# Performance work log

Measured on AMD Instinct MI355X. Metric: run time of the kernel, lower is better.

Reference implementation:

```python
import jax, jax.numpy as jnp
import numpy as np
from jax import lax

SIM_RATIO = 0.5
TAU = 1e-4
BN_EPS = 1e-5
COS_EPS = 1e-6
LEAKY_SLOPE = 0.01


def setup_inputs() -> dict:
    key = jax.random.key(0)
    ks = jax.random.split(key, 4)
    B, N, D = 2048, 50000, 128
    user_item_id = jax.random.randint(ks[0], (B, 2), 0, N, dtype=jnp.int64 if jax.config.jax_enable_x64 else jnp.int32).astype(jnp.int32)
    item_feature = jax.random.normal(ks[1], (B, 2 * D), dtype=jnp.float32)
    all_items = jax.random.normal(ks[2], (N, D), dtype=jnp.float32)
    # Linear(2D -> D) params (stored transposed: x @ W + b), BatchNorm1d affine params
    W = jax.random.normal(ks[3], (2 * D, D), dtype=jnp.float32) / np.float32(np.sqrt(2 * D))
    b = jnp.zeros((D,), jnp.float32)
    gamma = jnp.ones((D,), jnp.float32)
    beta = jnp.zeros((D,), jnp.float32)
    return {"user_item_id": user_item_id, "item_feature": item_feature,
            "all_items": all_items, "W": W, "b": b, "gamma": gamma, "beta": beta}


def _mlp(x, W, b, gamma, beta):
    # Linear + BatchNorm1d (training mode: batch stats, biased var) + LeakyReLU
    h = x @ W + b                                  # [B, D]
    mean = h.mean(axis=0)
    var = ((h - mean) ** 2).mean(axis=0)
    h = (h - mean) * lax.rsqrt(var + BN_EPS) * gamma + beta
    return jnp.where(h >= 0, h, LEAKY_SLOPE * h)


def reference(user_item_id, item_feature, all_items, W, b, gamma, beta):
    B = item_feature.shape[0]
    N = all_items.shape[0]
    h = _mlp(item_feature, W, b, gamma, beta)       # [B, D]
    scores = h @ all_items.T                         # [B, N]
    # hard gumbel-softmax, tau=1e-4
    g = jax.random.gumbel(jax.random.key(42), scores.shape, scores.dtype)
    soft = jax.nn.softmax((scores + g) / TAU, axis=-1)
    idx = jnp.argmax(soft, axis=-1)                  # [B]
    onehot = jax.nn.one_hot(idx, N, dtype=scores.dtype)
    probs = onehot + soft - lax.stop_gradient(soft)  # straight-through hard one-hot
    repl_feat = probs @ all_items                    # [B, D] (one-hot gather via matmul)
    repl_items = (jnp.arange(N, dtype=scores.dtype) * probs).sum(axis=1).astype(jnp.int32)
    orig_feat = all_items[user_item_id[:, 1]]        # [B, D]
    # cosine similarity along dim=1 with eps=1e-6 (torch semantics)
    dot = (orig_feat * repl_feat).sum(axis=1)
    n1 = jnp.maximum(jnp.linalg.norm(orig_feat, axis=1), COS_EPS)
    n2 = jnp.maximum(jnp.linalg.norm(repl_feat, axis=1), COS_EPS)
    sim = dot / (n1 * n2)
    sim = (sim + 1.0) / 2.0                          # regularize_similarity
    labels = jnp.full((B,), SIM_RATIO, dtype=sim.dtype)
    sim_loss = jnp.mean((sim - labels) ** 2)         # SimilarityMarginLoss ~ MSE to ratio
    return repl_items, sim_loss, sim.mean()
```

## Files before the change

kernel.cpp:

```cpp
#include <hip/hip_runtime.h>
#include <math.h>

#define TINYF 1.17549435e-38f
#define GMAX 16.0f
#define NTILES 1563
#define TPB 25

typedef __attribute__((ext_vector_type(8))) short bf16x8;
typedef __attribute__((ext_vector_type(4))) float f32x4;

__device__ __forceinline__ unsigned rotl32(unsigned x, int r) {
  return (x << r) | (x >> (32 - r));
}

__device__ __forceinline__ unsigned tf2x32_xor(unsigned x0, unsigned x1) {
  const unsigned k0 = 0u, k1 = 42u, k2 = 0x1BD11BF0u;
  x0 += k0; x1 += k1;
#define TFR(r) { x0 += x1; x1 = rotl32(x1, r); x1 ^= x0; }
  TFR(13) TFR(15) TFR(26) TFR(6)
  x0 += k1; x1 += k2 + 1u;
  TFR(17) TFR(29) TFR(16) TFR(24)
  x0 += k2; x1 += k0 + 2u;
  TFR(13) TFR(15) TFR(26) TFR(6)
  x0 += k0; x1 += k1 + 3u;
  TFR(17) TFR(29) TFR(16) TFR(24)
  x0 += k1; x1 += k2 + 4u;
  TFR(13) TFR(15) TFR(26) TFR(6)
  x0 += k2; x1 += k0 + 5u;
#undef TFR
  return x0 ^ x1;
}

__device__ __forceinline__ float gumbel_from_bits(unsigned bits) {
  float f = __uint_as_float((bits >> 9) | 0x3f800000u) - 1.0f;
  float u = fmaxf(f, TINYF);
  return -logf(-logf(u));
}

__device__ __forceinline__ unsigned ordf(float v) {
  unsigned b = __float_as_uint(v);
  return (b & 0x80000000u) ? ~b : (b | 0x80000000u);
}
__device__ __forceinline__ float unordf(unsigned u) {
  unsigned b = (u & 0x80000000u) ? (u & 0x7FFFFFFFu) : ~u;
  return __uint_as_float(b);
}

__device__ __forceinline__ unsigned short f2bf(float f) {
  unsigned u = __float_as_uint(f);
  unsigned r = u + 0x7FFFu + ((u >> 16) & 1u);
  return (unsigned short)(r >> 16);
}
__device__ __forceinline__ unsigned pk2(float a, float b) {
  return (unsigned)f2bf(a) | ((unsigned)f2bf(b) << 16);
}
__device__ __forceinline__ int bswz(int b) { return b ^ (((b >> 8) & 7) << 4); }

__device__ __attribute__((noinline)) void resolve_cand(
    int R, int J, float s, float ERRC,
    const float* __restrict__ hfin, const float* __restrict__ items,
    const float* __restrict__ V0,
    unsigned long long* __restrict__ rowslot, const volatile unsigned* hiw) {
  const unsigned hi0 = hiw[2 * R + 1];
  float tv = V0[R];
  if (hi0) tv = fmaxf(tv, unordf(hi0));
  const float thr2 = tv - ERRC;
  const float d = thr2 - s;
  const unsigned bits = tf2x32_xor(0u, (unsigned)R * 50000u + (unsigned)J);
  const float f = __uint_as_float((bits >> 9) | 0x3f800000u) - 1.0f;
  const float u = fmaxf(f, TINYF);
  const float thr_u = __expf(-__expf(-d)) * (1.0f - 2e-5f);
  if (u < thr_u) return;
  const float g = -logf(-logf(u));
  if (s + g < thr2) return;
  const float4* hp = (const float4*)(hfin + (size_t)R * 128);
  const float4* ap = (const float4*)(items + (size_t)J * 128);
  float4 a4 = {0.f, 0.f, 0.f, 0.f};
#pragma unroll
  for (int k = 0; k < 32; ++k) {
    float4 h = hp[k];
    float4 b = ap[k];
    a4.x = fmaf(h.x, b.x, a4.x);
    a4.y = fmaf(h.y, b.y, a4.y);
    a4.z = fmaf(h.z, b.z, a4.z);
    a4.w = fmaf(h.w, b.w, a4.w);
  }
  const float v = ((a4.x + a4.y) + (a4.z + a4.w)) + g;
  const unsigned ov = ordf(v);
  if (ov >= hiw[2 * R + 1]) {
    const unsigned long long pk =
        ((unsigned long long)ov << 32) | (0xFFFFFFFFu - (unsigned)J);
    atomicMax(&rowslot[R], pk);
  }
}

__global__ void k_hraw(const float* __restrict__ x, const float* __restrict__ W,
                       const float* __restrict__ b, float* __restrict__ hraw,
                       unsigned long long* __restrict__ rowslot,
                       float* __restrict__ norms) {
  __shared__ float sx[256];
  const int i = blockIdx.x;
  const int d = threadIdx.x;
  if (d == 0) {
    rowslot[i] = 0ull;
    if (i == 0) { norms[0] = 0.0f; norms[1] = 0.0f; }
  }
  sx[d] = x[i * 256 + d];
  sx[d + 128] = x[i * 256 + 128 + d];
  __syncthreads();
  double acc = 0.0;
  for (int k = 0; k < 256; ++k)
    acc = fma((double)sx[k], (double)W[k * 128 + d], acc);
  hraw[i * 128 + d] = (float)acc + b[d];
}

__global__ void k_bnstats(const float* __restrict__ hraw,
                          float* __restrict__ meanv, float* __restrict__ rsv) {
  __shared__ double red[256];
  const int d = blockIdx.x;
  const int t = threadIdx.x;
  double s = 0.0;
  for (int i = t; i < 2048; i += 256) s += (double)hraw[i * 128 + d];
  red[t] = s;
  __syncthreads();
  for (int off = 128; off > 0; off >>= 1) {
    if (t < off) red[t] += red[t + off];
    __syncthreads();
  }
  const float m = (float)(red[0] * (1.0 / 2048.0));
  __syncthreads();
  double v = 0.0;
  for (int i = t; i < 2048; i += 256) {
    float dd = __fsub_rn(hraw[i * 128 + d], m);
    v += (double)dd * (double)dd;
  }
  red[t] = v;
  __syncthreads();
  for (int off = 128; off > 0; off >>= 1) {
    if (t < off) red[t] += red[t + off];
    __syncthreads();
  }
  if (t == 0) {
    float var = (float)(red[0] * (1.0 / 2048.0));
    float vpe = __fadd_rn(var, 1e-5f);
    meanv[d] = m;
    rsv[d] = (float)(1.0 / sqrt((double)vpe));
  }
}

__global__ void k_apply(const float* __restrict__ hraw,
                        const float* __restrict__ meanv, const float* __restrict__ rsv,
                        const float* __restrict__ gamma, const float* __restrict__ beta,
                        float* __restrict__ hfin, unsigned short* __restrict__ hb,
                        float* __restrict__ norms) {
  __shared__ float red[256];
  const int t = threadIdx.x;
  const int idx = blockIdx.x * 256 + t;
  const int d = idx & 127;
  float h = hraw[idx];
  float hn = __fadd_rn(__fmul_rn(__fmul_rn(__fsub_rn(h, meanv[d]), rsv[d]), gamma[d]), beta[d]);
  float o = (hn >= 0.0f) ? hn : __fmul_rn(0.01f, hn);
  hfin[idx] = o;
  hb[idx] = f2bf(o);
  red[t] = o * o;
  __syncthreads();
  for (int off = 64; off > 0; off >>= 1) {
    if ((t & 127) < off) red[t] += red[t + off];
    __syncthreads();
  }
  if ((t & 127) == 0) atomicMax((unsigned*)&norms[0], __float_as_uint(red[t]));
}

__global__ void k_anorm(const float* __restrict__ items, float* __restrict__ norms) {
  __shared__ float red[4];
  const int t = threadIdx.x;
  int row = blockIdx.x * 32 + (t >> 3);
  if (row > 49999) row = 49999;
  const float4* p = (const float4*)(items + (size_t)row * 128 + (t & 7) * 16);
  float ss = 0.0f;
#pragma unroll
  for (int k = 0; k < 4; ++k) {
    float4 v = p[k];
    ss += v.x * v.x + v.y * v.y + v.z * v.z + v.w * v.w;
  }
  ss += __shfl_xor(ss, 1);
  ss += __shfl_xor(ss, 2);
  ss += __shfl_xor(ss, 4);
  ss = fmaxf(ss, __shfl_xor(ss, 8));
  ss = fmaxf(ss, __shfl_xor(ss, 16));
  ss = fmaxf(ss, __shfl_xor(ss, 32));
  if ((t & 63) == 0) red[t >> 6] = ss;
  __syncthreads();
  if (t == 0) {
    float mx = fmaxf(fmaxf(red[0], red[1]), fmaxf(red[2], red[3]));
    atomicMax((unsigned*)&norms[1], __float_as_uint(mx));
  }
}

__global__ __launch_bounds__(256, 4) void k_seed(const float* __restrict__ hfin,
                                                 const float* __restrict__ items,
                                                 float* __restrict__ V0) {
  __shared__ float red[4][256];
  const int t = threadIdx.x;
  const int rbase = blockIdx.x * 4;
  float best[4] = {-INFINITY, -INFINITY, -INFINITY, -INFINITY};
  for (int q = 0; q < 4; ++q) {
    const int j = t + 256 * q;
    float acc[4] = {0.0f, 0.0f, 0.0f, 0.0f};
    const float* ap = items + (size_t)j * 128;
    for (int km = 0; km < 8; ++km) {
#pragma unroll
      for (int e = 0; e < 4; ++e) {
        float4 a4 = *(const float4*)(ap + km * 16 + 4 * e);
#pragma unroll
        for (int p = 0; p < 4; ++p) {
          const float* hp = hfin + (rbase + p) * 128 + km * 16 + 4 * e;
          float4 h4 = *(const float4*)hp;
          acc[p] = fmaf(h4.x, a4.x, acc[p]);
          acc[p] = fmaf(h4.y, a4.y, acc[p]);
          acc[p] = fmaf(h4.z, a4.z, acc[p]);
          acc[p] = fmaf(h4.w, a4.w, acc[p]);
        }
      }
    }
#pragma unroll
    for (int p = 0; p < 4; ++p) {
      unsigned l = (unsigned)(rbase + p) * 50000u + (unsigned)j;
      float g = gumbel_from_bits(tf2x32_xor(0u, l));
      best[p] = fmaxf(best[p], acc[p] + g);
    }
  }
#pragma unroll
  for (int p = 0; p < 4; ++p) red[p][t] = best[p];
  __syncthreads();
  for (int off = 128; off > 0; off >>= 1) {
    if (t < off) {
#pragma unroll
      for (int p = 0; p < 4; ++p) red[p][t] = fmaxf(red[p][t], red[p][t + off]);
    }
    __syncthreads();
  }
  if (t < 4) V0[rbase + t] = red[t][0];
}

__global__ __launch_bounds__(256, 2) void k_screen(
    const unsigned short* __restrict__ hb, const float* __restrict__ hfin,
    const float* __restrict__ items, const float* __restrict__ V0,
    const float* __restrict__ norms, unsigned long long* __restrict__ rowslot) {
  __shared__ __align__(16) unsigned short Bs[2][32 * 128];
  __shared__ unsigned qk[4][128];
  __shared__ float qsh[4][128];

  const int t = threadIdx.x;
  const int w = t >> 6, l = t & 63;
  const int lg = l >> 4, lr = l & 15;
  const int rg = blockIdx.x >> 6;
  const int span = blockIdx.x & 63;
  const int r0 = rg * 128;
  const int r0w = r0 + w * 32;
  const int tile0 = span * TPB;
  int nt = NTILES - tile0;
  nt = nt < 0 ? 0 : (nt > TPB ? TPB : nt);
  if (nt == 0) return;

  const float ERRC = 0.004f * sqrtf(norms[0] * norms[1]) + 0.01f;
  const volatile unsigned* hiw = (const volatile unsigned*)rowslot;

  const unsigned short* aB0 = hb + (size_t)(r0w + lr) * 128 + lg * 8;
  bf16x8 Afrag[2][4];
#pragma unroll
  for (int kb = 0; kb < 4; ++kb) {
    Afrag[0][kb] = *(const bf16x8*)(aB0 + kb * 32);
    Afrag[1][kb] = *(const bf16x8*)(aB0 + 16 * 128 + kb * 32);
  }

  const int jl = t >> 3;
  const int c0 = (t & 7) * 16;
  float4 f0, f1, f2, f3;

  {
    const int Jg = min(tile0 * 32 + jl, 49999);
    const float4* src = (const float4*)(items + (size_t)Jg * 128 + c0);
    f0 = src[0]; f1 = src[1]; f2 = src[2]; f3 = src[3];
    uint4 A, B;
    A.x = pk2(f0.x, f0.y); A.y = pk2(f0.z, f0.w);
    A.z = pk2(f1.x, f1.y); A.w = pk2(f1.z, f1.w);
    B.x = pk2(f2.x, f2.y); B.y = pk2(f2.z, f2.w);
    B.z = pk2(f3.x, f3.y); B.w = pk2(f3.z, f3.w);
    const int byte0 = jl * 256 + c0 * 2;
    *(uint4*)((char*)Bs[0] + bswz(byte0)) = A;
    *(uint4*)((char*)Bs[0] + bswz(byte0 + 16)) = B;
  }
  if (nt > 1) {
    const int Jg = min((tile0 + 1) * 32 + jl, 49999);
    const float4* src = (const float4*)(items + (size_t)Jg * 128 + c0);
    f0 = src[0]; f1 = src[1]; f2 = src[2]; f3 = src[3];
  }
  __syncthreads();

  const unsigned long long lml = (1ull << l) - 1ull;
  unsigned qn = 0;
  float th1[2][4];

  int pb = 0;
  for (int it = 0; it < nt; ++it) {
    const int j0 = (tile0 + it) * 32;

    if ((it & 3) == 0) {
#pragma unroll
      for (int rt = 0; rt < 2; ++rt)
#pragma unroll
        for (int q = 0; q < 4; ++q) {
          const int R = r0w + rt * 16 + lg * 4 + q;
          const unsigned hi = hiw[2 * R + 1];
          float tv = V0[R];
          if (hi) tv = fmaxf(tv, unordf(hi));
          th1[rt][q] = tv - GMAX - ERRC;
        }
    }

    if (it + 1 < nt) {
      uint4 A, B;
      A.x = pk2(f0.x, f0.y); A.y = pk2(f0.z, f0.w);
      A.z = pk2(f1.x, f1.y); A.w = pk2(f1.z, f1.w);
      B.x = pk2(f2.x, f2.y); B.y = pk2(f2.z, f2.w);
      B.z = pk2(f3.x, f3.y); B.w = pk2(f3.z, f3.w);
      const int byte0 = jl * 256 + c0 * 2;
      *(uint4*)((char*)Bs[pb ^ 1] + bswz(byte0)) = A;
      *(uint4*)((char*)Bs[pb ^ 1] + bswz(byte0 + 16)) = B;
    }
    if (it + 2 < nt) {
      const int Jg = min((tile0 + it + 2) * 32 + jl, 49999);
      const float4* src = (const float4*)(items + (size_t)Jg * 128 + c0);
      f0 = src[0]; f1 = src[1]; f2 = src[2]; f3 = src[3];
    }

    f32x4 acc[2][2];
#pragma unroll
    for (int rt = 0; rt < 2; ++rt)
#pragma unroll
      for (int jt = 0; jt < 2; ++jt) acc[rt][jt] = (f32x4){0.f, 0.f, 0.f, 0.f};

#pragma unroll
    for (int kb = 0; kb < 4; ++kb) {
#pragma unroll
      for (int jt = 0; jt < 2; ++jt) {
        const int byte = (jt * 16 + lr) * 256 + kb * 64 + lg * 16;
        bf16x8 bfrag = *(const bf16x8*)((char*)Bs[pb] + bswz(byte));
        acc[0][jt] = __builtin_amdgcn_mfma_f32_16x16x32_bf16(Afrag[0][kb], bfrag, acc[0][jt], 0, 0, 0);
        acc[1][jt] = __builtin_amdgcn_mfma_f32_16x16x32_bf16(Afrag[1][kb], bfrag, acc[1][jt], 0, 0, 0);
      }
    }

#pragma unroll
    for (int rt = 0; rt < 2; ++rt)
#pragma unroll
      for (int q = 0; q < 4; ++q) {
        const float th = th1[rt][q];
#pragma unroll
        for (int jt = 0; jt < 2; ++jt) {
          const float s = acc[rt][jt][q];
          const int J = j0 + jt * 16 + lr;
          const bool c = (J < 50000) && (s >= th);
          const unsigned long long m = __ballot(c);
          if (m) {
            if (c) {
              const unsigned idx = qn + (unsigned)__popcll(m & lml);
              qk[w][idx] = ((unsigned)(rt * 16 + lg * 4 + q) << 16) | (unsigned)J;
              qsh[w][idx] = s;
            }
            qn += (unsigned)__popcll(m);
            if (qn >= 64) {
              for (unsigned i = (unsigned)l; i < qn; i += 64) {
                const unsigned key = qk[w][i];
                resolve_cand(r0w + (int)(key >> 16), (int)(key & 0xFFFFu),
                             qsh[w][i], ERRC, hfin, items, V0, rowslot, hiw);
              }
              qn = 0;
            }
          }
        }
      }

    __syncthreads();
    pb ^= 1;
  }

  for (unsigned i = (unsigned)l; i < qn; i += 64) {
    const unsigned key = qk[w][i];
    resolve_cand(r0w + (int)(key >> 16), (int)(key & 0xFFFFu),
                 qsh[w][i], ERRC, hfin, items, V0, rowslot, hiw);
  }
}

__global__ void k_final(const unsigned long long* __restrict__ rowslot,
                        const int* __restrict__ uid, const float* __restrict__ items,
                        float* __restrict__ dout, float* __restrict__ simv) {
  const int r = blockIdx.x;
  const int lane = threadIdx.x;
  const unsigned long long pk = rowslot[r];
  const int bi = (int)(0xFFFFFFFFu - (unsigned)pk);
  if (lane == 0) dout[r] = (float)bi;

  const int orig = uid[r * 2 + 1];
  float o1 = items[(size_t)orig * 128 + lane];
  float o2 = items[(size_t)orig * 128 + 64 + lane];
  float p1 = items[(size_t)bi * 128 + lane];
  float p2 = items[(size_t)bi * 128 + 64 + lane];
  float d = o1 * p1 + o2 * p2;
  float s1 = o1 * o1 + o2 * o2;
  float s2 = p1 * p1 + p2 * p2;
  for (int off = 32; off > 0; off >>= 1) {
    d += __shfl_down(d, off);
    s1 += __shfl_down(s1, off);
    s2 += __shfl_down(s2, off);
  }
  if (lane == 0) {
    float n1 = fmaxf(sqrtf(s1), 1e-6f);
    float n2 = fmaxf(sqrtf(s2), 1e-6f);
    float sim = d / (n1 * n2);
    simv[r] = (sim + 1.0f) * 0.5f;
  }
}

__global__ void k_reduce(const float* __restrict__ simv, float* __restrict__ dout) {
  __shared__ double rl[256];
  __shared__ double rs[256];
  const int t = threadIdx.x;
  double L = 0.0, S = 0.0;
  for (int i = t; i < 2048; i += 256) {
    double s = (double)simv[i];
    double dd = s - 0.5;
    L += dd * dd;
    S += s;
  }
  rl[t] = L; rs[t] = S;
  __syncthreads();
  for (int off = 128; off > 0; off >>= 1) {
    if (t < off) { rl[t] += rl[t + off]; rs[t] += rs[t + off]; }
    __syncthreads();
  }
  if (t == 0) {
    dout[2048] = (float)(rl[0] * (1.0 / 2048.0));
    dout[2049] = (float)(rs[0] * (1.0 / 2048.0));
  }
}

extern "C" void kernel_launch(void* const* d_in, const int* in_sizes, int n_in,
                              void* d_out, int out_size, void* d_ws, size_t ws_size,
                              hipStream_t stream) {
  const int* uid = (const int*)d_in[0];
  const float* xfeat = (const float*)d_in[1];
  const float* items = (const float*)d_in[2];
  const float* W = (const float*)d_in[3];
  const float* bias = (const float*)d_in[4];
  const float* gamma = (const float*)d_in[5];
  const float* beta = (const float*)d_in[6];

  float* ws = (float*)d_ws;
  float* hraw = ws;
  float* hfin = ws + 262144;
  float* meanv = ws + 524288;
  float* rsv = ws + 524416;
  float* V0 = ws + 524544;
  float* simv = ws + 526592;
  float* norms = ws + 528640;
  unsigned long long* rowslot =
      (unsigned long long*)(ws + 528642);
  unsigned short* hb = (unsigned short*)(ws + 532740);
  float* dout = (float*)d_out;

  hipLaunchKernelGGL(k_hraw, dim3(2048), dim3(128), 0, stream, xfeat, W, bias, hraw, rowslot, norms);
  hipLaunchKernelGGL(k_bnstats, dim3(128), dim3(256), 0, stream, hraw, meanv, rsv);
  hipLaunchKernelGGL(k_apply, dim3(1024), dim3(256), 0, stream, hraw, meanv, rsv, gamma, beta, hfin, hb, norms);
  hipLaunchKernelGGL(k_anorm, dim3(1563), dim3(256), 0, stream, items, norms);
  hipLaunchKernelGGL(k_seed, dim3(512), dim3(256), 0, stream, hfin, items, V0);
  hipLaunchKernelGGL(k_screen, dim3(1024), dim3(256), 0, stream, hb, hfin, items, V0, norms, rowslot);
  hipLaunchKernelGGL(k_final, dim3(2048), dim3(64), 0, stream, rowslot, uid, items, dout, simv);
  hipLaunchKernelGGL(k_reduce, dim3(1), dim3(256), 0, stream, simv, dout);
}
```

Before: 411.0 us.

## Pre-convert items to bf16 and stage screen tiles via direct global-to-LDS loads

Adds a kernel that converts the item table to bf16 once per call into workspace. The screening kernel then streams tiles with global_load_lds straight into the swizzled shared buffer, instead of loading fp32 into registers, packing, and writing to LDS. This halves the bytes streamed per tile and frees VGPRs and VALU work in the hot loop. The cost is an extra conversion pass over the 50000x128 table each call, plus a fallback path that is taken when the workspace is too small.

```diff
diff --git a/kernel.cpp b/kernel.cpp
--- a/kernel.cpp
+++ b/kernel.cpp
@@ -94,6 +94,17 @@
   }
 }
 
+__global__ void k_bconv(const float* __restrict__ items,
+                        unsigned short* __restrict__ ib) {
+  const int e = (blockIdx.x * 256 + threadIdx.x) * 8;
+  const float4 a = *(const float4*)(items + e);
+  const float4 b = *(const float4*)(items + e + 4);
+  uint4 o;
+  o.x = pk2(a.x, a.y); o.y = pk2(a.z, a.w);
+  o.z = pk2(b.x, b.y); o.w = pk2(b.z, b.w);
+  *(uint4*)(ib + e) = o;
+}
+
 __global__ void k_hraw(const float* __restrict__ x, const float* __restrict__ W,
                        const float* __restrict__ b, float* __restrict__ hraw,
                        unsigned long long* __restrict__ rowslot,
@@ -243,9 +254,10 @@
   if (t < 4) V0[rbase + t] = red[t][0];
 }
 
-__global__ __launch_bounds__(256, 2) void k_screen(
+__global__ __launch_bounds__(256, 2) void k_screen_dma(
     const unsigned short* __restrict__ hb, const float* __restrict__ hfin,
-    const float* __restrict__ items, const float* __restrict__ V0,
+    const float* __restrict__ items, const unsigned short* __restrict__ ib,
+    const float* __restrict__ V0,
     const float* __restrict__ norms, unsigned long long* __restrict__ rowslot) {
   __shared__ __align__(16) unsigned short Bs[2][32 * 128];
   __shared__ unsigned qk[4][128];
@@ -274,28 +286,26 @@
     Afrag[1][kb] = *(const bf16x8*)(aB0 + 16 * 128 + kb * 32);
   }
 
-  const int jl = t >> 3;
-  const int c0 = (t & 7) * 16;
-  float4 f0, f1, f2, f3;
-
-  {
-    const int Jg = min(tile0 * 32 + jl, 49999);
-    const float4* src = (const float4*)(items + (size_t)Jg * 128 + c0);
-    f0 = src[0]; f1 = src[1]; f2 = src[2]; f3 = src[3];
-    uint4 A, B;
-    A.x = pk2(f0.x, f0.y); A.y = pk2(f0.z, f0.w);
-    A.z = pk2(f1.x, f1.y); A.w = pk2(f1.z, f1.w);
-    B.x = pk2(f2.x, f2.y); B.y = pk2(f2.z, f2.w);
-    B.z = pk2(f3.x, f3.y); B.w = pk2(f3.z, f3.w);
-    const int byte0 = jl * 256 + c0 * 2;
-    *(uint4*)((char*)Bs[0] + bswz(byte0)) = A;
-    *(uint4*)((char*)Bs[0] + bswz(byte0 + 16)) = B;
-  }
-  if (nt > 1) {
-    const int Jg = min((tile0 + 1) * 32 + jl, 49999);
-    const float4* src = (const float4*)(items + (size_t)Jg * 128 + c0);
-    f0 = src[0]; f1 = src[1]; f2 = src[2]; f3 = src[3];
-  }
+  const int o0 = w * 2048 + l * 16;
+  const int row0 = o0 >> 8, col0 = o0 & 255;
+  const int o1 = o0 + 1024;
+  const int row1 = o1 >> 8, col1 = o1 & 255;
+  const int sc0 = col0 ^ ((row0 & 7) << 4);
+  const int sc1 = col1 ^ ((row1 & 7) << 4);
+
+#define STAGE_TILE(tl, buf)                                                    \
+  {                                                                            \
+    const int Jg0 = min((tl) * 32 + row0, 49999);                              \
+    const int Jg1 = min((tl) * 32 + row1, 49999);                              \
+    __builtin_amdgcn_global_load_lds(                                          \
+        (const unsigned int*)((const char*)ib + (size_t)Jg0 * 256 + sc0),      \
+        (unsigned int*)((char*)Bs[buf] + w * 2048), 16, 0, 0);                 \
+    __builtin_amdgcn_global_load_lds(                                          \
+        (const unsigned int*)((const char*)ib + (size_t)Jg1 * 256 + sc1),      \
+        (unsigned int*)((char*)Bs[buf] + w * 2048 + 1024), 16, 0, 0);          \
+  }
+
+  STAGE_TILE(tile0, 0)
   __syncthreads();
 
   const unsigned long long lml = (1ull << l) - 1ull;
@@ -305,6 +315,8 @@
   int pb = 0;
   for (int it = 0; it < nt; ++it) {
     const int j0 = (tile0 + it) * 32;
+
+    if (it + 1 < nt) STAGE_TILE(tile0 + it + 1, pb ^ 1)
 
     if ((it & 3) == 0) {
 #pragma unroll
@@ -317,22 +329,6 @@
           if (hi) tv = fmaxf(tv, unordf(hi));
           th1[rt][q] = tv - GMAX - ERRC;
         }
-    }
-
-    if (it + 1 < nt) {
-      uint4 A, B;
-      A.x = pk2(f0.x, f0.y); A.y = pk2(f0.z, f0.w);
-      A.z = pk2(f1.x, f1.y); A.w = pk2(f1.z, f1.w);
-      B.x = pk2(f2.x, f2.y); B.y = pk2(f2.z, f2.w);
-      B.z = pk2(f3.x, f3.y); B.w = pk2(f3.z, f3.w);
-      const int byte0 = jl * 256 + c0 * 2;
-      *(uint4*)((char*)Bs[pb ^ 1] + bswz(byte0)) = A;
-      *(uint4*)((char*)Bs[pb ^ 1] + bswz(byte0 + 16)) = B;
-    }
-    if (it + 2 < nt) {
-      const int Jg = min((tile0 + it + 2) * 32 + jl, 49999);
-      const float4* src = (const float4*)(items + (size_t)Jg * 128 + c0);
-      f0 = src[0]; f1 = src[1]; f2 = src[2]; f3 = src[3];
     }
 
     f32x4 acc[2][2];
@@ -391,6 +387,157 @@
     resolve_cand(r0w + (int)(key >> 16), (int)(key & 0xFFFFu),
                  qsh[w][i], ERRC, hfin, items, V0, rowslot, hiw);
   }
+#undef STAGE_TILE
+}
+
+__global__ __launch_bounds__(256, 2) void k_screen_reg(
+    const unsigned short* __restrict__ hb, const float* __restrict__ hfin,
+    const float* __restrict__ items, const float* __restrict__ V0,
+    const float* __restrict__ norms, unsigned long long* __restrict__ rowslot) {
+  __shared__ __align__(16) unsigned short Bs[2][32 * 128];
+  __shared__ unsigned qk[4][128];
+  __shared__ float qsh[4][128];
+
+  const int t = threadIdx.x;
+  const int w = t >> 6, l = t & 63;
+  const int lg = l >> 4, lr = l & 15;
+  const int rg = blockIdx.x >> 6;
+  const int span = blockIdx.x & 63;
+  const int r0 = rg * 128;
+  const int r0w = r0 + w * 32;
+  const int tile0 = span * TPB;
+  int nt = NTILES - tile0;
+  nt = nt < 0 ? 0 : (nt > TPB ? TPB : nt);
+  if (nt == 0) return;
+
+  const float ERRC = 0.004f * sqrtf(norms[0] * norms[1]) + 0.01f;
+  const volatile unsigned* hiw = (const volatile unsigned*)rowslot;
+
+  const unsigned short* aB0 = hb + (size_t)(r0w + lr) * 128 + lg * 8;
+  bf16x8 Afrag[2][4];
+#pragma unroll
+  for (int kb = 0; kb < 4; ++kb) {
+    Afrag[0][kb] = *(const bf16x8*)(aB0 + kb * 32);
+    Afrag[1][kb] = *(const bf16x8*)(aB0 + 16 * 128 + kb * 32);
+  }
+
+  const int jl = t >> 3;
+  const int c0 = (t & 7) * 16;
+  float4 f0, f1, f2, f3;
+
+  {
+    const int Jg = min(tile0 * 32 + jl, 49999);
+    const float4* src = (const float4*)(items + (size_t)Jg * 128 + c0);
+    f0 = src[0]; f1 = src[1]; f2 = src[2]; f3 = src[3];
+    uint4 A, B;
+    A.x = pk2(f0.x, f0.y); A.y = pk2(f0.z, f0.w);
+    A.z = pk2(f1.x, f1.y); A.w = pk2(f1.z, f1.w);
+    B.x = pk2(f2.x, f2.y); B.y = pk2(f2.z, f2.w);
+    B.z = pk2(f3.x, f3.y); B.w = pk2(f3.z, f3.w);
+    const int byte0 = jl * 256 + c0 * 2;
+    *(uint4*)((char*)Bs[0] + bswz(byte0)) = A;
+    *(uint4*)((char*)Bs[0] + bswz(byte0 + 16)) = B;
+  }
+  if (nt > 1) {
+    const int Jg = min((tile0 + 1) * 32 + jl, 49999);
+    const float4* src = (const float4*)(items + (size_t)Jg * 128 + c0);
+    f0 = src[0]; f1 = src[1]; f2 = src[2]; f3 = src[3];
+  }
+  __syncthreads();
+
+  const unsigned long long lml = (1ull << l) - 1ull;
+  unsigned qn = 0;
+  float th1[2][4];
+
+  int pb = 0;
+  for (int it = 0; it < nt; ++it) {
+    const int j0 = (tile0 + it) * 32;
+
+    if ((it & 3) == 0) {
+#pragma unroll
+      for (int rt = 0; rt < 2; ++rt)
+#pragma unroll
+        for (int q = 0; q < 4; ++q) {
+          const int R = r0w + rt * 16 + lg * 4 + q;
+          const unsigned hi = hiw[2 * R + 1];
+          float tv = V0[R];
+          if (hi) tv = fmaxf(tv, unordf(hi));
+          th1[rt][q] = tv - GMAX - ERRC;
+        }
+    }
+
+    if (it + 1 < nt) {
+      uint4 A, B;
+      A.x = pk2(f0.x, f0.y); A.y = pk2(f0.z, f0.w);
+      A.z = pk2(f1.x, f1.y); A.w = pk2(f1.z, f1.w);
+      B.x = pk2(f2.x, f2.y); B.y = pk2(f2.z, f2.w);
+      B.z = pk2(f3.x, f3.y); B.w = pk2(f3.z, f3.w);
+      const int byte0 = jl * 256 + c0 * 2;
+      *(uint4*)((char*)Bs[pb ^ 1] + bswz(byte0)) = A;
+      *(uint4*)((char*)Bs[pb ^ 1] + bswz(byte0 + 16)) = B;
+    }
+    if (it + 2 < nt) {
+      const int Jg = min((tile0 + it + 2) * 32 + jl, 49999);
+      const float4* src = (const float4*)(items + (size_t)Jg * 128 + c0);
+      f0 = src[0]; f1 = src[1]; f2 = src[2]; f3 = src[3];
+    }
+
+    f32x4 acc[2][2];
+#pragma unroll
+    for (int rt = 0; rt < 2; ++rt)
+#pragma unroll
+      for (int jt = 0; jt < 2; ++jt) acc[rt][jt] = (f32x4){0.f, 0.f, 0.f, 0.f};
+
+#pragma unroll
+    for (int kb = 0; kb < 4; ++kb) {
+#pragma unroll
+      for (int jt = 0; jt < 2; ++jt) {
+        const int byte = (jt * 16 + lr) * 256 + kb * 64 + lg * 16;
+        bf16x8 bfrag = *(const bf16x8*)((char*)Bs[pb] + bswz(byte));
+        acc[0][jt] = __builtin_amdgcn_mfma_f32_16x16x32_bf16(Afrag[0][kb], bfrag, acc[0][jt], 0, 0, 0);
+        acc[1][jt] = __builtin_amdgcn_mfma_f32_16x16x32_bf16(Afrag[1][kb], bfrag, acc[1][jt], 0, 0, 0);
+      }
+    }
+
+#pragma unroll
+    for (int rt = 0; rt < 2; ++rt)
+#pragma unroll
+      for (int q = 0; q < 4; ++q) {
+        const float th = th1[rt][q];
+#pragma unroll
+        for (int jt = 0; jt < 2; ++jt) {
+          const float s = acc[rt][jt][q];
+          const int J = j0 + jt * 16 + lr;
+          const bool c = (J < 50000) && (s >= th);
+          const unsigned long long m = __ballot(c);
+          if (m) {
+            if (c) {
+              const unsigned idx = qn + (unsigned)__popcll(m & lml);
+              qk[w][idx] = ((unsigned)(rt * 16 + lg * 4 + q) << 16) | (unsigned)J;
+              qsh[w][idx] = s;
+            }
+            qn += (unsigned)__popcll(m);
+            if (qn >= 64) {
+              for (unsigned i = (unsigned)l; i < qn; i += 64) {
+                const unsigned key = qk[w][i];
+                resolve_cand(r0w + (int)(key >> 16), (int)(key & 0xFFFFu),
+                             qsh[w][i], ERRC, hfin, items, V0, rowslot, hiw);
+              }
+              qn = 0;
+            }
+          }
+        }
+      }
+
+    __syncthreads();
+    pb ^= 1;
+  }
+
+  for (unsigned i = (unsigned)l; i < qn; i += 64) {
+    const unsigned key = qk[w][i];
+    resolve_cand(r0w + (int)(key >> 16), (int)(key & 0xFFFFu),
+                 qsh[w][i], ERRC, hfin, items, V0, rowslot, hiw);
+  }
 }
 
 __global__ void k_final(const unsigned long long* __restrict__ rowslot,
@@ -468,14 +615,22 @@
   unsigned long long* rowslot =
       (unsigned long long*)(ws + 528642);
   unsigned short* hb = (unsigned short*)(ws + 532740);
+  unsigned short* ib = (unsigned short*)(ws + 663812);
   float* dout = (float*)d_out;
 
+  const bool big_ws = ws_size >= (size_t)15455248;
+
+  if (big_ws)
+    hipLaunchKernelGGL(k_bconv, dim3(3125), dim3(256), 0, stream, items, ib);
   hipLaunchKernelGGL(k_hraw, dim3(2048), dim3(128), 0, stream, xfeat, W, bias, hraw, rowslot, norms);
   hipLaunchKernelGGL(k_bnstats, dim3(128), dim3(256), 0, stream, hraw, meanv, rsv);
   hipLaunchKernelGGL(k_apply, dim3(1024), dim3(256), 0, stream, hraw, meanv, rsv, gamma, beta, hfin, hb, norms);
   hipLaunchKernelGGL(k_anorm, dim3(1563), dim3(256), 0, stream, items, norms);
   hipLaunchKernelGGL(k_seed, dim3(512), dim3(256), 0, stream, hfin, items, V0);
-  hipLaunchKernelGGL(k_screen, dim3(1024), dim3(256), 0, stream, hb, hfin, items, V0, norms, rowslot);
+  if (big_ws)
+    hipLaunchKernelGGL(k_screen_dma, dim3(1024), dim3(256), 0, stream, hb, hfin, items, ib, V0, norms, rowslot);
+  else
+    hipLaunchKernelGGL(k_screen_reg, dim3(1024), dim3(256), 0, stream, hb, hfin, items, V0, norms, rowslot);
   hipLaunchKernelGGL(k_final, dim3(2048), dim3(64), 0, stream, rowslot, uid, items, dout, simv);
   hipLaunchKernelGGL(k_reduce, dim3(1), dim3(256), 0, stream, simv, dout);
 }
```

Measured after the change: 412.4 us. No clear change (+0.4%).

## Precast items to bf16 once and stream tiles via direct global-to-LDS loads

Applied to the files above, without the earlier changes.

Replaces the item-norm kernel with one that also writes a bf16 copy of the item table while computing the max norm. The screening kernel then loads pre-swizzled bf16 tiles straight into LDS with global_load_lds, instead of loading fp32 into registers and packing per tile. The row tile per block is halved (16 rows per wave, 64 per block) and the grid doubles, so each block does less MFMA work per B tile and thresholds are refreshed every iteration via a shuffle. This trades an extra pass writing about 12.8MB of bf16 for half the bytes read per tile and lower register pressure, but each tile is now re-read by twice as many blocks.

```diff
diff --git a/kernel.cpp b/kernel.cpp
--- a/kernel.cpp
+++ b/kernel.cpp
@@ -114,6 +114,43 @@
   hraw[i * 128 + d] = (float)acc + b[d];
 }
 
+__global__ void k_bca(const float* __restrict__ items,
+                      unsigned short* __restrict__ ib,
+                      float* __restrict__ norms) {
+  __shared__ float red[4];
+  const int t = threadIdx.x;
+  const int row = blockIdx.x * 32 + (t >> 3);
+  const int rc = row > 49999 ? 49999 : row;
+  const int c = (t & 7) * 16;
+  const float4* p = (const float4*)(items + (size_t)rc * 128 + c);
+  const float4 v0 = p[0], v1 = p[1], v2 = p[2], v3 = p[3];
+  float ss = v0.x * v0.x + v0.y * v0.y + v0.z * v0.z + v0.w * v0.w +
+             v1.x * v1.x + v1.y * v1.y + v1.z * v1.z + v1.w * v1.w +
+             v2.x * v2.x + v2.y * v2.y + v2.z * v2.z + v2.w * v2.w +
+             v3.x * v3.x + v3.y * v3.y + v3.z * v3.z + v3.w * v3.w;
+  if (row <= 49999) {
+    uint4 o0, o1;
+    o0.x = pk2(v0.x, v0.y); o0.y = pk2(v0.z, v0.w);
+    o0.z = pk2(v1.x, v1.y); o0.w = pk2(v1.z, v1.w);
+    o1.x = pk2(v2.x, v2.y); o1.y = pk2(v2.z, v2.w);
+    o1.z = pk2(v3.x, v3.y); o1.w = pk2(v3.z, v3.w);
+    uint4* dst = (uint4*)(ib + (size_t)row * 128 + c);
+    dst[0] = o0; dst[1] = o1;
+  }
+  ss += __shfl_xor(ss, 1);
+  ss += __shfl_xor(ss, 2);
+  ss += __shfl_xor(ss, 4);
+  ss = fmaxf(ss, __shfl_xor(ss, 8));
+  ss = fmaxf(ss, __shfl_xor(ss, 16));
+  ss = fmaxf(ss, __shfl_xor(ss, 32));
+  if ((t & 63) == 0) red[t >> 6] = ss;
+  __syncthreads();
+  if (t == 0) {
+    float mx = fmaxf(fmaxf(red[0], red[1]), fmaxf(red[2], red[3]));
+    atomicMax((unsigned*)&norms[1], __float_as_uint(mx));
+  }
+}
+
 __global__ void k_bnstats(const float* __restrict__ hraw,
                           float* __restrict__ meanv, float* __restrict__ rsv) {
   __shared__ double red[256];
@@ -169,32 +206,6 @@
     __syncthreads();
   }
   if ((t & 127) == 0) atomicMax((unsigned*)&norms[0], __float_as_uint(red[t]));
-}
-
-__global__ void k_anorm(const float* __restrict__ items, float* __restrict__ norms) {
-  __shared__ float red[4];
-  const int t = threadIdx.x;
-  int row = blockIdx.x * 32 + (t >> 3);
-  if (row > 49999) row = 49999;
-  const float4* p = (const float4*)(items + (size_t)row * 128 + (t & 7) * 16);
-  float ss = 0.0f;
-#pragma unroll
-  for (int k = 0; k < 4; ++k) {
-    float4 v = p[k];
-    ss += v.x * v.x + v.y * v.y + v.z * v.z + v.w * v.w;
-  }
-  ss += __shfl_xor(ss, 1);
-  ss += __shfl_xor(ss, 2);
-  ss += __shfl_xor(ss, 4);
-  ss = fmaxf(ss, __shfl_xor(ss, 8));
-  ss = fmaxf(ss, __shfl_xor(ss, 16));
-  ss = fmaxf(ss, __shfl_xor(ss, 32));
-  if ((t & 63) == 0) red[t >> 6] = ss;
-  __syncthreads();
-  if (t == 0) {
-    float mx = fmaxf(fmaxf(red[0], red[1]), fmaxf(red[2], red[3]));
-    atomicMax((unsigned*)&norms[1], __float_as_uint(mx));
-  }
 }
 
 __global__ __launch_bounds__(256, 4) void k_seed(const float* __restrict__ hfin,
@@ -245,7 +256,8 @@
 
 __global__ __launch_bounds__(256, 2) void k_screen(
     const unsigned short* __restrict__ hb, const float* __restrict__ hfin,
-    const float* __restrict__ items, const float* __restrict__ V0,
+    const float* __restrict__ items, const unsigned short* __restrict__ ib,
+    const float* __restrict__ V0,
     const float* __restrict__ norms, unsigned long long* __restrict__ rowslot) {
   __shared__ __align__(16) unsigned short Bs[2][32 * 128];
   __shared__ unsigned qk[4][128];
@@ -256,8 +268,7 @@
   const int lg = l >> 4, lr = l & 15;
   const int rg = blockIdx.x >> 6;
   const int span = blockIdx.x & 63;
-  const int r0 = rg * 128;
-  const int r0w = r0 + w * 32;
+  const int r0w = rg * 64 + w * 16;
   const int tile0 = span * TPB;
   int nt = NTILES - tile0;
   nt = nt < 0 ? 0 : (nt > TPB ? TPB : nt);
@@ -267,120 +278,93 @@
   const volatile unsigned* hiw = (const volatile unsigned*)rowslot;
 
   const unsigned short* aB0 = hb + (size_t)(r0w + lr) * 128 + lg * 8;
-  bf16x8 Afrag[2][4];
-#pragma unroll
-  for (int kb = 0; kb < 4; ++kb) {
-    Afrag[0][kb] = *(const bf16x8*)(aB0 + kb * 32);
-    Afrag[1][kb] = *(const bf16x8*)(aB0 + 16 * 128 + kb * 32);
-  }
-
-  const int jl = t >> 3;
-  const int c0 = (t & 7) * 16;
-  float4 f0, f1, f2, f3;
-
-  {
-    const int Jg = min(tile0 * 32 + jl, 49999);
-    const float4* src = (const float4*)(items + (size_t)Jg * 128 + c0);
-    f0 = src[0]; f1 = src[1]; f2 = src[2]; f3 = src[3];
-    uint4 A, B;
-    A.x = pk2(f0.x, f0.y); A.y = pk2(f0.z, f0.w);
-    A.z = pk2(f1.x, f1.y); A.w = pk2(f1.z, f1.w);
-    B.x = pk2(f2.x, f2.y); B.y = pk2(f2.z, f2.w);
-    B.z = pk2(f3.x, f3.y); B.w = pk2(f3.z, f3.w);
-    const int byte0 = jl * 256 + c0 * 2;
-    *(uint4*)((char*)Bs[0] + bswz(byte0)) = A;
-    *(uint4*)((char*)Bs[0] + bswz(byte0 + 16)) = B;
-  }
-  if (nt > 1) {
-    const int Jg = min((tile0 + 1) * 32 + jl, 49999);
-    const float4* src = (const float4*)(items + (size_t)Jg * 128 + c0);
-    f0 = src[0]; f1 = src[1]; f2 = src[2]; f3 = src[3];
-  }
+  bf16x8 Afrag[4];
+#pragma unroll
+  for (int kb = 0; kb < 4; ++kb) Afrag[kb] = *(const bf16x8*)(aB0 + kb * 32);
+
+  const int o0 = w * 2048 + l * 16;
+  const int row0 = o0 >> 8, col0 = o0 & 255;
+  const int o1 = o0 + 1024;
+  const int row1 = o1 >> 8, col1 = o1 & 255;
+  const int sc0 = col0 ^ ((row0 & 7) << 4);
+  const int sc1 = col1 ^ ((row1 & 7) << 4);
+
+#define STAGE_TILE(tl, buf)                                                    \
+  {                                                                            \
+    const int Jg0 = min((tl) * 32 + row0, 49999);                              \
+    const int Jg1 = min((tl) * 32 + row1, 49999);                              \
+    __builtin_amdgcn_global_load_lds(                                          \
+        (const unsigned int*)((const char*)ib + (size_t)Jg0 * 256 + sc0),      \
+        (unsigned int*)((char*)Bs[buf] + w * 2048), 16, 0, 0);                 \
+    __builtin_amdgcn_global_load_lds(                                          \
+        (const unsigned int*)((const char*)ib + (size_t)Jg1 * 256 + sc1),      \
+        (unsigned int*)((char*)Bs[buf] + w * 2048 + 1024), 16, 0, 0);          \
+  }
+
+  STAGE_TILE(tile0, 0)
   __syncthreads();
 
   const unsigned long long lml = (1ull << l) - 1ull;
   unsigned qn = 0;
-  float th1[2][4];
 
   int pb = 0;
   for (int it = 0; it < nt; ++it) {
     const int j0 = (tile0 + it) * 32;
 
-    if ((it & 3) == 0) {
-#pragma unroll
-      for (int rt = 0; rt < 2; ++rt)
-#pragma unroll
-        for (int q = 0; q < 4; ++q) {
-          const int R = r0w + rt * 16 + lg * 4 + q;
-          const unsigned hi = hiw[2 * R + 1];
-          float tv = V0[R];
-          if (hi) tv = fmaxf(tv, unordf(hi));
-          th1[rt][q] = tv - GMAX - ERRC;
-        }
-    }
-
-    if (it + 1 < nt) {
-      uint4 A, B;
-      A.x = pk2(f0.x, f0.y); A.y = pk2(f0.z, f0.w);
-      A.z = pk2(f1.x, f1.y); A.w = pk2(f1.z, f1.w);
-      B.x = pk2(f2.x, f2.y); B.y = pk2(f2.z, f2.w);
-      B.z = pk2(f3.x, f3.y); B.w = pk2(f3.z, f3.w);
-      const int byte0 = jl * 256 + c0 * 2;
-      *(uint4*)((char*)Bs[pb ^ 1] + bswz(byte0)) = A;
-      *(uint4*)((char*)Bs[pb ^ 1] + bswz(byte0 + 16)) = B;
-    }
-    if (it + 2 < nt) {
-      const int Jg = min((tile0 + it + 2) * 32 + jl, 49999);
-      const float4* src = (const float4*)(items + (size_t)Jg * 128 + c0);
-      f0 = src[0]; f1 = src[1]; f2 = src[2]; f3 = src[3];
-    }
-
-    f32x4 acc[2][2];
-#pragma unroll
-    for (int rt = 0; rt < 2; ++rt)
-#pragma unroll
-      for (int jt = 0; jt < 2; ++jt) acc[rt][jt] = (f32x4){0.f, 0.f, 0.f, 0.f};
-
+    if (it + 1 < nt) STAGE_TILE(tile0 + it + 1, pb ^ 1)
+
+    float tvl = 0.0f;
+    if (l < 16) {
+      const int R = r0w + l;
+      const unsigned hi = hiw[2 * R + 1];
+      tvl = V0[R];
+      if (hi) tvl = fmaxf(tvl, unordf(hi));
+    }
+    float th1[4];
+#pragma unroll
+    for (int q = 0; q < 4; ++q)
+      th1[q] = __shfl(tvl, lg * 4 + q) - GMAX - ERRC;
+
+    f32x4 acc[2];
+    acc[0] = (f32x4){0.f, 0.f, 0.f, 0.f};
+    acc[1] = (f32x4){0.f, 0.f, 0.f, 0.f};
 #pragma unroll
     for (int kb = 0; kb < 4; ++kb) {
 #pragma unroll
       for (int jt = 0; jt < 2; ++jt) {
         const int byte = (jt * 16 + lr) * 256 + kb * 64 + lg * 16;
         bf16x8 bfrag = *(const bf16x8*)((char*)Bs[pb] + bswz(byte));
-        acc[0][jt] = __builtin_amdgcn_mfma_f32_16x16x32_bf16(Afrag[0][kb], bfrag, acc[0][jt], 0, 0, 0);
-        acc[1][jt] = __builtin_amdgcn_mfma_f32_16x16x32_bf16(Afrag[1][kb], bfrag, acc[1][jt], 0, 0, 0);
+        acc[jt] = __builtin_amdgcn_mfma_f32_16x16x32_bf16(Afrag[kb], bfrag, acc[jt], 0, 0, 0);
       }
     }
 
 #pragma unroll
-    for (int rt = 0; rt < 2; ++rt)
-#pragma unroll
-      for (int q = 0; q < 4; ++q) {
-        const float th = th1[rt][q];
-#pragma unroll
-        for (int jt = 0; jt < 2; ++jt) {
-          const float s = acc[rt][jt][q];
-          const int J = j0 + jt * 16 + lr;
-          const bool c = (J < 50000) && (s >= th);
-          const unsigned long long m = __ballot(c);
-          if (m) {
-            if (c) {
-              const unsigned idx = qn + (unsigned)__popcll(m & lml);
-              qk[w][idx] = ((unsigned)(rt * 16 + lg * 4 + q) << 16) | (unsigned)J;
-              qsh[w][idx] = s;
+    for (int q = 0; q < 4; ++q) {
+      const float th = th1[q];
+#pragma unroll
+      for (int jt = 0; jt < 2; ++jt) {
+        const float s = acc[jt][q];
+        const int J = j0 + jt * 16 + lr;
+        const bool c = (J < 50000) && (s >= th);
+        const unsigned long long m = __ballot(c);
+        if (m) {
+          if (c) {
+            const unsigned idx = qn + (unsigned)__popcll(m & lml);
+            qk[w][idx] = ((unsigned)(lg * 4 + q) << 16) | (unsigned)J;
+            qsh[w][idx] = s;
+          }
+          qn += (unsigned)__popcll(m);
+          if (qn >= 64) {
+            for (unsigned i = (unsigned)l; i < qn; i += 64) {
+              const unsigned key = qk[w][i];
+              resolve_cand(r0w + (int)(key >> 16), (int)(key & 0xFFFFu),
+                           qsh[w][i], ERRC, hfin, items, V0, rowslot, hiw);
             }
-            qn += (unsigned)__popcll(m);
-            if (qn >= 64) {
-              for (unsigned i = (unsigned)l; i < qn; i += 64) {
-                const unsigned key = qk[w][i];
-                resolve_cand(r0w + (int)(key >> 16), (int)(key & 0xFFFFu),
-                             qsh[w][i], ERRC, hfin, items, V0, rowslot, hiw);
-              }
-              qn = 0;
-            }
+            qn = 0;
           }
         }
       }
+    }
 
     __syncthreads();
     pb ^= 1;
@@ -391,6 +375,7 @@
     resolve_cand(r0w + (int)(key >> 16), (int)(key & 0xFFFFu),
                  qsh[w][i], ERRC, hfin, items, V0, rowslot, hiw);
   }
+#undef STAGE_TILE
 }
 
 __global__ void k_final(const unsigned long long* __restrict__ rowslot,
@@ -468,14 +453,15 @@
   unsigned long long* rowslot =
       (unsigned long long*)(ws + 528642);
   unsigned short* hb = (unsigned short*)(ws + 532740);
+  unsigned short* ib = (unsigned short*)(ws + 663812);
   float* dout = (float*)d_out;
 
   hipLaunchKernelGGL(k_hraw, dim3(2048), dim3(128), 0, stream, xfeat, W, bias, hraw, rowslot, norms);
+  hipLaunchKernelGGL(k_bca, dim3(1563), dim3(256), 0, stream, items, ib, norms);
   hipLaunchKernelGGL(k_bnstats, dim3(128), dim3(256), 0, stream, hraw, meanv, rsv);
   hipLaunchKernelGGL(k_apply, dim3(1024), dim3(256), 0, stream, hraw, meanv, rsv, gamma, beta, hfin, hb, norms);
-  hipLaunchKernelGGL(k_anorm, dim3(1563), dim3(256), 0, stream, items, norms);
   hipLaunchKernelGGL(k_seed, dim3(512), dim3(256), 0, stream, hfin, items, V0);
-  hipLaunchKernelGGL(k_screen, dim3(1024), dim3(256), 0, stream, hb, hfin, items, V0, norms, rowslot);
+  hipLaunchKernelGGL(k_screen, dim3(2048), dim3(256), 0, stream, hb, hfin, items, ib, V0, norms, rowslot);
   hipLaunchKernelGGL(k_final, dim3(2048), dim3(64), 0, stream, rowslot, uid, items, dout, simv);
   hipLaunchKernelGGL(k_reduce, dim3(1), dim3(256), 0, stream, simv, dout);
 }
```

Result: no change. 407.2 us (-0.9%).
